# Performance work log

Hardware: AMD Instinct MI355X
Metric: run time of the kernel (lower is better)

The kernel has to match this reference:

```python
import jax, jax.numpy as jnp
import numpy as np
import math

D_MODEL = 512
N_HEADS = 8
MAX_SEQ_LEN = 4096
DENSITY = 0.3


def _make_random_mask(key, seq_len, density=DENSITY):
    # rand < density, symmetrized via (m + m.T)/2, clamped to [0,1], diag = 1
    u = jax.random.uniform(key, (seq_len, seq_len), dtype=jnp.float32)
    m = (u < density).astype(jnp.float32)
    m = jnp.clip((m + m.T) * 0.5, 0.0, 1.0)
    return m.at[jnp.diag_indices(seq_len)].set(1.0)


def setup_inputs() -> dict:
    key = jax.random.key(0)
    ks = jax.random.split(key, 10)
    B, T, C = 2, 4096, D_MODEL
    scale = 1.0 / math.sqrt(C)
    x = jax.random.normal(ks[0], (B, T, C), dtype=jnp.float32)
    mask = _make_random_mask(ks[1], MAX_SEQ_LEN)[:T, :T]
    # Linear weights stored as (in, out): y = x @ W + b
    Wq = jax.random.normal(ks[2], (C, C), dtype=jnp.float32) * scale
    Wk = jax.random.normal(ks[3], (C, C), dtype=jnp.float32) * scale
    Wv = jax.random.normal(ks[4], (C, C), dtype=jnp.float32) * scale
    Wo = jax.random.normal(ks[5], (C, C), dtype=jnp.float32) * scale
    bq = jax.random.normal(ks[6], (C,), dtype=jnp.float32) * scale
    bk = jax.random.normal(ks[7], (C,), dtype=jnp.float32) * scale
    bv = jax.random.normal(ks[8], (C,), dtype=jnp.float32) * scale
    bo = jax.random.normal(ks[9], (C,), dtype=jnp.float32) * scale
    return {"x": x, "mask": mask, "Wq": Wq, "bq": bq, "Wk": Wk, "bk": bk,
            "Wv": Wv, "bv": bv, "Wo": Wo, "bo": bo}


def reference(x, mask, Wq, bq, Wk, bk, Wv, bv, Wo, bo):
    B, T, C = x.shape
    H = N_HEADS
    dk = C // H
    q = (x @ Wq + bq).reshape(B, T, H, dk)
    k = (x @ Wk + bk).reshape(B, T, H, dk)
    v = (x @ Wv + bv).reshape(B, T, H, dk)
    # scores: [B, H, T, T]
    attn = jnp.einsum('bthd,bshd->bhts', q, k) / math.sqrt(dk)
    attn = attn * mask[None, None, :, :]  # multiplicative mask PRE-softmax
    p = jax.nn.softmax(attn, axis=-1)
    out = jnp.einsum('bhts,bshd->bthd', p, v).reshape(B, T, C)
    return out @ Wo + bo
```

## Files before the change

kernel.cpp:

```cpp
#include <hip/hip_runtime.h>
#include <math.h>

#define D_MODEL 512
#define N_HEADS 8
#define DK 64

typedef __attribute__((ext_vector_type(8))) short short8;
typedef __attribute__((ext_vector_type(4))) float f32x4;

typedef __attribute__((address_space(1))) const unsigned as1_uint;
typedef __attribute__((address_space(3))) unsigned as3_uint;

__device__ __forceinline__ unsigned short f2bf(float f) {
    unsigned u = __builtin_bit_cast(unsigned, f);
    u = (u + 0x7fff + ((u >> 16) & 1)) >> 16;
    return (unsigned short)u;
}

__global__ __launch_bounds__(256) void cvt_x_kernel(const float* __restrict__ x,
                                                    unsigned short* __restrict__ xb, int n8)
{
    int i = blockIdx.x * 256 + threadIdx.x;
    if (i >= n8) return;
    float4 a = ((const float4*)x)[i * 2];
    float4 b = ((const float4*)x)[i * 2 + 1];
    short8 o;
    o[0] = f2bf(a.x); o[1] = f2bf(a.y); o[2] = f2bf(a.z); o[3] = f2bf(a.w);
    o[4] = f2bf(b.x); o[5] = f2bf(b.y); o[6] = f2bf(b.z); o[7] = f2bf(b.w);
    ((short8*)xb)[i] = o;
}

__global__ __launch_bounds__(256) void cvt_wt_kernel(const float* __restrict__ W,
                                                     unsigned short* __restrict__ Wt)
{
    __shared__ float tile[64][65];
    int t = threadIdx.x;
    int c0 = blockIdx.x * 64;
    int r0 = blockIdx.y * 64;
    #pragma unroll
    for (int i = 0; i < 16; i++) {
        int e = i * 256 + t, r = e >> 6, c = e & 63;
        tile[c][r] = W[(size_t)(r0 + r) * D_MODEL + c0 + c];
    }
    __syncthreads();
    #pragma unroll
    for (int i = 0; i < 16; i++) {
        int e = i * 256 + t, n = e >> 6, kk = e & 63;
        Wt[(size_t)(c0 + n) * D_MODEL + r0 + kk] = f2bf(tile[n][kk]);
    }
}

template<int MODE>
__global__ __launch_bounds__(512) void gemm_mfma_kernel(
    const unsigned short* __restrict__ A, const unsigned short* __restrict__ Bt,
    const float* __restrict__ bias, void* __restrict__ outp, int M, int T)
{
    constexpr int K = D_MODEL;
    __shared__ unsigned short As[2][128 * 32];
    __shared__ unsigned short Bs[2][128 * 32];
    int t = threadIdx.x;
    int lane = t & 63, w = t >> 6;
    int ql = lane & 15, kg = lane >> 4;
    int m0 = blockIdx.y * 128, n0 = blockIdx.x * 128;
    int wm = w >> 2, wn = w & 3;

    const unsigned short* srcA = A + (size_t)(m0 + (t >> 2)) * K + (t & 3) * 8;
    const unsigned short* srcB = Bt + (size_t)(n0 + (t >> 2)) * K + (t & 3) * 8;

    f32x4 acc[4][2];
    #pragma unroll
    for (int i = 0; i < 4; i++)
        #pragma unroll
        for (int j = 0; j < 2; j++) { f32x4 z = {0.f, 0.f, 0.f, 0.f}; acc[i][j] = z; }

    constexpr int NIT = K / 32;
    int cur = 0;
    __builtin_amdgcn_global_load_lds((as1_uint*)(srcA),
        (as3_uint*)((char*)&As[0][0] + w * 1024), 16, 0, 0);
    __builtin_amdgcn_global_load_lds((as1_uint*)(srcB),
        (as3_uint*)((char*)&Bs[0][0] + w * 1024), 16, 0, 0);
    __syncthreads();

    for (int it = 0; it < NIT; ++it) {
        if (it + 1 < NIT) {
            int k0 = (it + 1) * 32;
            __builtin_amdgcn_global_load_lds((as1_uint*)(srcA + k0),
                (as3_uint*)((char*)&As[cur ^ 1][0] + w * 1024), 16, 0, 0);
            __builtin_amdgcn_global_load_lds((as1_uint*)(srcB + k0),
                (as3_uint*)((char*)&Bs[cur ^ 1][0] + w * 1024), 16, 0, 0);
        }
        short8 af[4], bfr[2];
        #pragma unroll
        for (int fm = 0; fm < 4; fm++)
            af[fm] = *(const short8*)((const char*)&As[cur][0] + (wm * 64 + fm * 16 + ql) * 64 + kg * 16);
        #pragma unroll
        for (int fn = 0; fn < 2; fn++)
            bfr[fn] = *(const short8*)((const char*)&Bs[cur][0] + (wn * 32 + fn * 16 + ql) * 64 + kg * 16);
        #pragma unroll
        for (int fm = 0; fm < 4; fm++)
            #pragma unroll
            for (int fn = 0; fn < 2; fn++) {
                if (MODE == 3)
                    acc[fm][fn] = __builtin_amdgcn_mfma_f32_16x16x32_bf16(bfr[fn], af[fm], acc[fm][fn], 0, 0, 0);
                else
                    acc[fm][fn] = __builtin_amdgcn_mfma_f32_16x16x32_bf16(af[fm], bfr[fn], acc[fm][fn], 0, 0, 0);
            }
        __syncthreads();
        cur ^= 1;
    }

    #pragma unroll
    for (int fm = 0; fm < 4; fm++) {
        #pragma unroll
        for (int fn = 0; fn < 2; fn++) {
            if (MODE == 3) {
                int m = m0 + wm * 64 + fm * 16 + ql;
                int b = m / T, tt = m % T;
                #pragma unroll
                for (int r = 0; r < 4; r++) {
                    int n = n0 + wn * 32 + fn * 16 + kg * 4 + r;
                    float val = acc[fm][fn][r] + bias[n];
                    int h = n >> 6, d = n & 63;
                    ((unsigned short*)outp)[((size_t)(b * N_HEADS + h) * DK + d) * T + tt] = f2bf(val);
                }
            } else {
                int n = n0 + wn * 32 + fn * 16 + ql;
                float bn = bias[n];
                #pragma unroll
                for (int r = 0; r < 4; r++) {
                    int m = m0 + wm * 64 + fm * 16 + kg * 4 + r;
                    float val = acc[fm][fn][r] + bn;
                    if (MODE == 0) {
                        ((float*)outp)[(size_t)m * D_MODEL + n] = val;
                    } else {
                        if (MODE == 1) val *= 0.125f * 1.44269504089f;
                        int b = m / T, tt = m % T;
                        int h = n >> 6, d = n & 63;
                        ((unsigned short*)outp)[((size_t)(b * N_HEADS + h) * T + tt) * DK + d] = f2bf(val);
                    }
                }
            }
        }
    }
}

__global__ __launch_bounds__(256) void attn_mfma_kernel(
    const unsigned short* __restrict__ q, const unsigned short* __restrict__ k,
    const unsigned short* __restrict__ v, const float* __restrict__ mask,
    unsigned short* __restrict__ out, int B, int T)
{
    __shared__ unsigned short Ks[2][64 * 64];
    __shared__ unsigned short Vt[2][64 * 64];
    __shared__ unsigned short Ps[4][16 * 64];

    int t = threadIdx.x;
    int lane = t & 63, w = t >> 6;
    int ql = lane & 15, kg = lane >> 4;
    int bh = blockIdx.x;
    int qt = blockIdx.y;
    int h = bh & (N_HEADS - 1), b = bh >> 3;
    int qr0 = qt * 64;

    const char* kbase = (const char*)(k + (size_t)bh * T * DK);
    const char* vbase = (const char*)(v + (size_t)bh * DK * T);
    const float* mrow = mask + (size_t)(qr0 + w * 16 + ql) * T + kg * 4;

    short8 qf[2];
    {
        const unsigned short* qrow = q + ((size_t)bh * T + qr0 + w * 16 + ql) * DK + kg * 8;
        qf[0] = *(const short8*)(qrow);
        qf[1] = *(const short8*)(qrow + 32);
    }

    f32x4 oacc[4];
    #pragma unroll
    for (int c = 0; c < 4; c++) { f32x4 z = {0.f, 0.f, 0.f, 0.f}; oacc[c] = z; }
    float lacc = 0.f;

    #pragma unroll
    for (int i = 0; i < 2; i++) {
        int off = (i * 256 + t) * 16;
        int row = off >> 7;
        short8 kv = *(const short8*)(kbase + off);
        short8 vv = *(const short8*)(vbase + (size_t)row * (T * 2) + (off & 127));
        *(short8*)((char*)&Ks[0][0] + (off ^ ((row & 7) << 4))) = kv;
        *(short8*)((char*)&Vt[0][0] + (off ^ ((row & 7) << 4))) = vv;
    }

    int ntiles = T / 64;
    for (int kt = 0; kt < ntiles; kt++) {
        __syncthreads();
        int cur = kt & 1;
        bool havenext = (kt + 1) < ntiles;

        float4 mv[4];
        const float* mp = mrow + (size_t)kt * 64;
        #pragma unroll
        for (int c = 0; c < 4; c++) mv[c] = *(const float4*)(mp + c * 16);

        short8 kreg[2], vreg[2];
        if (havenext) {
            #pragma unroll
            for (int i = 0; i < 2; i++) {
                int off = (i * 256 + t) * 16;
                int row = off >> 7;
                kreg[i] = *(const short8*)(kbase + (size_t)(kt + 1) * 8192 + off);
                vreg[i] = *(const short8*)(vbase + (size_t)row * (T * 2) + (size_t)(kt + 1) * 128 + (off & 127));
            }
        }

        f32x4 sacc[4];
        #pragma unroll
        for (int c = 0; c < 4; c++) { f32x4 z = {0.f, 0.f, 0.f, 0.f}; sacc[c] = z; }
        __builtin_amdgcn_s_setprio(1);
        #pragma unroll
        for (int ks = 0; ks < 2; ks++) {
            #pragma unroll
            for (int c = 0; c < 4; c++) {
                int row = c * 16 + ql;
                short8 kf = *(const short8*)((const char*)&Ks[cur][0] +
                            ((row * 128 + ks * 64 + kg * 16) ^ ((row & 7) << 4)));
                sacc[c] = __builtin_amdgcn_mfma_f32_16x16x32_bf16(kf, qf[ks], sacc[c], 0, 0, 0);
            }
        }
        __builtin_amdgcn_s_setprio(0);

        #pragma unroll
        for (int c = 0; c < 4; c++) {
            float p0 = __builtin_amdgcn_exp2f(sacc[c][0] * mv[c].x);
            float p1 = __builtin_amdgcn_exp2f(sacc[c][1] * mv[c].y);
            float p2 = __builtin_amdgcn_exp2f(sacc[c][2] * mv[c].z);
            float p3 = __builtin_amdgcn_exp2f(sacc[c][3] * mv[c].w);
            lacc += (p0 + p1) + (p2 + p3);
            unsigned lo, hi;
            asm("v_cvt_pk_bf16_f32 %0, %1, %2" : "=v"(lo) : "v"(p0), "v"(p1));
            asm("v_cvt_pk_bf16_f32 %0, %1, %2" : "=v"(hi) : "v"(p2), "v"(p3));
            int byteoff = (ql * 128 + (c * 16 + kg * 4) * 2) ^ ((ql & 7) << 4);
            uint2 pr = { lo, hi };
            *(uint2*)((char*)&Ps[w][0] + byteoff) = pr;
        }

        __builtin_amdgcn_s_setprio(1);
        #pragma unroll
        for (int ks = 0; ks < 2; ks++) {
            short8 pa = *(const short8*)((const char*)&Ps[w][0] +
                        ((ql * 128 + ks * 64 + kg * 16) ^ ((ql & 7) << 4)));
            #pragma unroll
            for (int c2 = 0; c2 < 4; c2++) {
                int rowd = c2 * 16 + ql;
                short8 vb = *(const short8*)((const char*)&Vt[cur][0] +
                            ((rowd * 128 + ks * 64 + kg * 16) ^ ((rowd & 7) << 4)));
                oacc[c2] = __builtin_amdgcn_mfma_f32_16x16x32_bf16(pa, vb, oacc[c2], 0, 0, 0);
            }
        }
        __builtin_amdgcn_s_setprio(0);

        if (havenext) {
            #pragma unroll
            for (int i = 0; i < 2; i++) {
                int off = (i * 256 + t) * 16;
                int row = off >> 7;
                *(short8*)((char*)&Ks[cur ^ 1][0] + (off ^ ((row & 7) << 4))) = kreg[i];
                *(short8*)((char*)&Vt[cur ^ 1][0] + (off ^ ((row & 7) << 4))) = vreg[i];
            }
        }
    }

    lacc += __shfl_xor(lacc, 16, 64);
    lacc += __shfl_xor(lacc, 32, 64);
    float linv[4];
    #pragma unroll
    for (int r = 0; r < 4; r++) linv[r] = 1.0f / __shfl(lacc, kg * 4 + r, 64);
    #pragma unroll
    for (int r = 0; r < 4; r++) {
        size_t rowo = ((size_t)b * T + qr0 + w * 16 + kg * 4 + r) * D_MODEL + h * DK;
        #pragma unroll
        for (int c2 = 0; c2 < 4; c2++)
            out[rowo + c2 * 16 + ql] = f2bf(oacc[c2][r] * linv[r]);
    }
}

extern "C" void kernel_launch(void* const* d_in, const int* in_sizes, int n_in,
                              void* d_out, int out_size, void* d_ws, size_t ws_size,
                              hipStream_t stream) {
    const float* x    = (const float*)d_in[0];
    const float* mask = (const float*)d_in[1];
    const float* Wq   = (const float*)d_in[2];
    const float* bq   = (const float*)d_in[3];
    const float* Wk   = (const float*)d_in[4];
    const float* bk   = (const float*)d_in[5];
    const float* Wv   = (const float*)d_in[6];
    const float* bv   = (const float*)d_in[7];
    const float* Wo   = (const float*)d_in[8];
    const float* bo   = (const float*)d_in[9];

    int T = (int)(sqrt((double)in_sizes[1]) + 0.5);
    int C = D_MODEL;
    int B = in_sizes[0] / (T * C);
    int M = B * T;

    size_t MK = (size_t)M * C;
    unsigned short* xb  = (unsigned short*)d_ws;
    unsigned short* Wtq = xb + MK;
    unsigned short* Wtk = Wtq + (size_t)C * C;
    unsigned short* Wtv = Wtk + (size_t)C * C;
    unsigned short* Wto = Wtv + (size_t)C * C;
    unsigned short* qb  = Wto + (size_t)C * C;
    unsigned short* kb  = qb + MK;
    unsigned short* vb  = kb + MK;
    unsigned short* attb = vb + MK;

    int n8 = (int)(MK / 8);
    cvt_x_kernel<<<(n8 + 255) / 256, 256, 0, stream>>>(x, xb, n8);
    dim3 wtg(C / 64, C / 64, 1);
    cvt_wt_kernel<<<wtg, 256, 0, stream>>>(Wq, Wtq);
    cvt_wt_kernel<<<wtg, 256, 0, stream>>>(Wk, Wtk);
    cvt_wt_kernel<<<wtg, 256, 0, stream>>>(Wv, Wtv);
    cvt_wt_kernel<<<wtg, 256, 0, stream>>>(Wo, Wto);

    dim3 gg(C / 128, M / 128, 1);
    gemm_mfma_kernel<1><<<gg, 512, 0, stream>>>(xb, Wtq, bq, qb, M, T);
    gemm_mfma_kernel<2><<<gg, 512, 0, stream>>>(xb, Wtk, bk, kb, M, T);
    gemm_mfma_kernel<3><<<gg, 512, 0, stream>>>(xb, Wtv, bv, vb, M, T);

    dim3 ga(B * N_HEADS, T / 64, 1);
    attn_mfma_kernel<<<ga, 256, 0, stream>>>(qb, kb, vb, mask, attb, B, T);

    gemm_mfma_kernel<0><<<gg, 512, 0, stream>>>(attb, Wto, bo, d_out, M, T);
}
```

Before: 241.7 us.

## Double query rows per attention block and stream K/V tiles directly into LDS

Each wave now handles 32 query rows instead of 16, so every K/V tile loaded into shared memory feeds twice as many MFMAs and global K/V traffic per output row is halved. The grid along the query dimension shrinks by two. K/V prefetch now uses global_load_lds direct-to-LDS loads with pre-swizzled source addresses instead of register staging and LDS stores. The trade-off is fewer blocks (occupancy and load balance across CUs), more registers for the doubled accumulators, and twice the mask loads per wave. Correctness of the async LDS loads depends on the existing __syncthreads ordering.

```diff
diff --git a/kernel.cpp b/kernel.cpp
--- a/kernel.cpp
+++ b/kernel.cpp
@@ -151,7 +151,7 @@
 {
     __shared__ unsigned short Ks[2][64 * 64];
     __shared__ unsigned short Vt[2][64 * 64];
-    __shared__ unsigned short Ps[4][16 * 64];
+    __shared__ unsigned short Ps[4][32 * 64];
 
     int t = threadIdx.x;
     int lane = t & 63, w = t >> 6;
@@ -159,59 +159,77 @@
     int bh = blockIdx.x;
     int qt = blockIdx.y;
     int h = bh & (N_HEADS - 1), b = bh >> 3;
-    int qr0 = qt * 64;
+    int qr0 = qt * 128;
 
     const char* kbase = (const char*)(k + (size_t)bh * T * DK);
     const char* vbase = (const char*)(v + (size_t)bh * DK * T);
-    const float* mrow = mask + (size_t)(qr0 + w * 16 + ql) * T + kg * 4;
-
-    short8 qf[2];
-    {
-        const unsigned short* qrow = q + ((size_t)bh * T + qr0 + w * 16 + ql) * DK + kg * 8;
-        qf[0] = *(const short8*)(qrow);
-        qf[1] = *(const short8*)(qrow + 32);
-    }
-
-    f32x4 oacc[4];
-    #pragma unroll
-    for (int c = 0; c < 4; c++) { f32x4 z = {0.f, 0.f, 0.f, 0.f}; oacc[c] = z; }
-    float lacc = 0.f;
-
-    #pragma unroll
-    for (int i = 0; i < 2; i++) {
-        int off = (i * 256 + t) * 16;
-        int row = off >> 7;
-        short8 kv = *(const short8*)(kbase + off);
-        short8 vv = *(const short8*)(vbase + (size_t)row * (T * 2) + (off & 127));
-        *(short8*)((char*)&Ks[0][0] + (off ^ ((row & 7) << 4))) = kv;
-        *(short8*)((char*)&Vt[0][0] + (off ^ ((row & 7) << 4))) = vv;
-    }
+
+    int lin0 = w * 1024 + lane * 16;
+    int lin1 = 4096 + lin0;
+    int row0 = lin0 >> 7, row1 = lin1 >> 7;
+    int sw0 = (row0 & 7) << 4, sw1 = (row1 & 7) << 4;
+    const char* gK0 = kbase + (lin0 ^ sw0);
+    const char* gK1 = kbase + (lin1 ^ sw1);
+    const char* gV0 = vbase + (size_t)row0 * (2 * T) + ((lin0 & 127) ^ sw0);
+    const char* gV1 = vbase + (size_t)row1 * (2 * T) + ((lin1 & 127) ^ sw1);
+
+    short8 qfr[2][2];
+    #pragma unroll
+    for (int qf = 0; qf < 2; qf++) {
+        const unsigned short* qrow = q + ((size_t)bh * T + qr0 + w * 32 + qf * 16 + ql) * DK + kg * 8;
+        qfr[qf][0] = *(const short8*)(qrow);
+        qfr[qf][1] = *(const short8*)(qrow + 32);
+    }
+
+    const float* mrow0 = mask + (size_t)(qr0 + w * 32 + ql) * T + kg * 4;
+    const float* mrow1 = mrow0 + (size_t)16 * T;
+
+    f32x4 oacc[2][4];
+    #pragma unroll
+    for (int qf = 0; qf < 2; qf++)
+        #pragma unroll
+        for (int c = 0; c < 4; c++) { f32x4 z = {0.f, 0.f, 0.f, 0.f}; oacc[qf][c] = z; }
+    float lacc0 = 0.f, lacc1 = 0.f;
+
+    __builtin_amdgcn_global_load_lds((as1_uint*)gK0, (as3_uint*)((char*)&Ks[0][0] + w * 1024), 16, 0, 0);
+    __builtin_amdgcn_global_load_lds((as1_uint*)gK1, (as3_uint*)((char*)&Ks[0][0] + 4096 + w * 1024), 16, 0, 0);
+    __builtin_amdgcn_global_load_lds((as1_uint*)gV0, (as3_uint*)((char*)&Vt[0][0] + w * 1024), 16, 0, 0);
+    __builtin_amdgcn_global_load_lds((as1_uint*)gV1, (as3_uint*)((char*)&Vt[0][0] + 4096 + w * 1024), 16, 0, 0);
 
     int ntiles = T / 64;
     for (int kt = 0; kt < ntiles; kt++) {
         __syncthreads();
         int cur = kt & 1;
-        bool havenext = (kt + 1) < ntiles;
-
-        float4 mv[4];
-        const float* mp = mrow + (size_t)kt * 64;
-        #pragma unroll
-        for (int c = 0; c < 4; c++) mv[c] = *(const float4*)(mp + c * 16);
-
-        short8 kreg[2], vreg[2];
-        if (havenext) {
-            #pragma unroll
-            for (int i = 0; i < 2; i++) {
-                int off = (i * 256 + t) * 16;
-                int row = off >> 7;
-                kreg[i] = *(const short8*)(kbase + (size_t)(kt + 1) * 8192 + off);
-                vreg[i] = *(const short8*)(vbase + (size_t)row * (T * 2) + (size_t)(kt + 1) * 128 + (off & 127));
-            }
-        }
-
-        f32x4 sacc[4];
-        #pragma unroll
-        for (int c = 0; c < 4; c++) { f32x4 z = {0.f, 0.f, 0.f, 0.f}; sacc[c] = z; }
+
+        float4 mv0[4], mv1[4];
+        {
+            const float* mp0 = mrow0 + (size_t)kt * 64;
+            const float* mp1 = mrow1 + (size_t)kt * 64;
+            #pragma unroll
+            for (int c = 0; c < 4; c++) {
+                mv0[c] = *(const float4*)(mp0 + c * 16);
+                mv1[c] = *(const float4*)(mp1 + c * 16);
+            }
+        }
+
+        if (kt + 1 < ntiles) {
+            size_t ko = (size_t)(kt + 1) * 8192;
+            size_t vo = (size_t)(kt + 1) * 128;
+            __builtin_amdgcn_global_load_lds((as1_uint*)(gK0 + ko),
+                (as3_uint*)((char*)&Ks[cur ^ 1][0] + w * 1024), 16, 0, 0);
+            __builtin_amdgcn_global_load_lds((as1_uint*)(gK1 + ko),
+                (as3_uint*)((char*)&Ks[cur ^ 1][0] + 4096 + w * 1024), 16, 0, 0);
+            __builtin_amdgcn_global_load_lds((as1_uint*)(gV0 + vo),
+                (as3_uint*)((char*)&Vt[cur ^ 1][0] + w * 1024), 16, 0, 0);
+            __builtin_amdgcn_global_load_lds((as1_uint*)(gV1 + vo),
+                (as3_uint*)((char*)&Vt[cur ^ 1][0] + 4096 + w * 1024), 16, 0, 0);
+        }
+
+        f32x4 sacc[2][4];
+        #pragma unroll
+        for (int qf = 0; qf < 2; qf++)
+            #pragma unroll
+            for (int c = 0; c < 4; c++) { f32x4 z = {0.f, 0.f, 0.f, 0.f}; sacc[qf][c] = z; }
         __builtin_amdgcn_s_setprio(1);
         #pragma unroll
         for (int ks = 0; ks < 2; ks++) {
@@ -220,63 +238,71 @@
                 int row = c * 16 + ql;
                 short8 kf = *(const short8*)((const char*)&Ks[cur][0] +
                             ((row * 128 + ks * 64 + kg * 16) ^ ((row & 7) << 4)));
-                sacc[c] = __builtin_amdgcn_mfma_f32_16x16x32_bf16(kf, qf[ks], sacc[c], 0, 0, 0);
+                sacc[0][c] = __builtin_amdgcn_mfma_f32_16x16x32_bf16(kf, qfr[0][ks], sacc[0][c], 0, 0, 0);
+                sacc[1][c] = __builtin_amdgcn_mfma_f32_16x16x32_bf16(kf, qfr[1][ks], sacc[1][c], 0, 0, 0);
             }
         }
         __builtin_amdgcn_s_setprio(0);
 
         #pragma unroll
         for (int c = 0; c < 4; c++) {
-            float p0 = __builtin_amdgcn_exp2f(sacc[c][0] * mv[c].x);
-            float p1 = __builtin_amdgcn_exp2f(sacc[c][1] * mv[c].y);
-            float p2 = __builtin_amdgcn_exp2f(sacc[c][2] * mv[c].z);
-            float p3 = __builtin_amdgcn_exp2f(sacc[c][3] * mv[c].w);
-            lacc += (p0 + p1) + (p2 + p3);
+            float p0 = __builtin_amdgcn_exp2f(sacc[0][c][0] * mv0[c].x);
+            float p1 = __builtin_amdgcn_exp2f(sacc[0][c][1] * mv0[c].y);
+            float p2 = __builtin_amdgcn_exp2f(sacc[0][c][2] * mv0[c].z);
+            float p3 = __builtin_amdgcn_exp2f(sacc[0][c][3] * mv0[c].w);
+            lacc0 += (p0 + p1) + (p2 + p3);
             unsigned lo, hi;
             asm("v_cvt_pk_bf16_f32 %0, %1, %2" : "=v"(lo) : "v"(p0), "v"(p1));
             asm("v_cvt_pk_bf16_f32 %0, %1, %2" : "=v"(hi) : "v"(p2), "v"(p3));
             int byteoff = (ql * 128 + (c * 16 + kg * 4) * 2) ^ ((ql & 7) << 4);
             uint2 pr = { lo, hi };
             *(uint2*)((char*)&Ps[w][0] + byteoff) = pr;
+
+            float q0 = __builtin_amdgcn_exp2f(sacc[1][c][0] * mv1[c].x);
+            float q1 = __builtin_amdgcn_exp2f(sacc[1][c][1] * mv1[c].y);
+            float q2 = __builtin_amdgcn_exp2f(sacc[1][c][2] * mv1[c].z);
+            float q3 = __builtin_amdgcn_exp2f(sacc[1][c][3] * mv1[c].w);
+            lacc1 += (q0 + q1) + (q2 + q3);
+            unsigned lo1, hi1;
+            asm("v_cvt_pk_bf16_f32 %0, %1, %2" : "=v"(lo1) : "v"(q0), "v"(q1));
+            asm("v_cvt_pk_bf16_f32 %0, %1, %2" : "=v"(hi1) : "v"(q2), "v"(q3));
+            uint2 pr1 = { lo1, hi1 };
+            *(uint2*)((char*)&Ps[w][0] + 2048 + byteoff) = pr1;
         }
 
         __builtin_amdgcn_s_setprio(1);
         #pragma unroll
         for (int ks = 0; ks < 2; ks++) {
-            short8 pa = *(const short8*)((const char*)&Ps[w][0] +
-                        ((ql * 128 + ks * 64 + kg * 16) ^ ((ql & 7) << 4)));
+            int pboff = (ql * 128 + ks * 64 + kg * 16) ^ ((ql & 7) << 4);
+            short8 pa0 = *(const short8*)((const char*)&Ps[w][0] + pboff);
+            short8 pa1 = *(const short8*)((const char*)&Ps[w][0] + 2048 + pboff);
             #pragma unroll
             for (int c2 = 0; c2 < 4; c2++) {
                 int rowd = c2 * 16 + ql;
                 short8 vb = *(const short8*)((const char*)&Vt[cur][0] +
                             ((rowd * 128 + ks * 64 + kg * 16) ^ ((rowd & 7) << 4)));
-                oacc[c2] = __builtin_amdgcn_mfma_f32_16x16x32_bf16(pa, vb, oacc[c2], 0, 0, 0);
+                oacc[0][c2] = __builtin_amdgcn_mfma_f32_16x16x32_bf16(pa0, vb, oacc[0][c2], 0, 0, 0);
+                oacc[1][c2] = __builtin_amdgcn_mfma_f32_16x16x32_bf16(pa1, vb, oacc[1][c2], 0, 0, 0);
             }
         }
         __builtin_amdgcn_s_setprio(0);
-
-        if (havenext) {
-            #pragma unroll
-            for (int i = 0; i < 2; i++) {
-                int off = (i * 256 + t) * 16;
-                int row = off >> 7;
-                *(short8*)((char*)&Ks[cur ^ 1][0] + (off ^ ((row & 7) << 4))) = kreg[i];
-                *(short8*)((char*)&Vt[cur ^ 1][0] + (off ^ ((row & 7) << 4))) = vreg[i];
-            }
-        }
-    }
-
-    lacc += __shfl_xor(lacc, 16, 64);
-    lacc += __shfl_xor(lacc, 32, 64);
-    float linv[4];
-    #pragma unroll
-    for (int r = 0; r < 4; r++) linv[r] = 1.0f / __shfl(lacc, kg * 4 + r, 64);
-    #pragma unroll
-    for (int r = 0; r < 4; r++) {
-        size_t rowo = ((size_t)b * T + qr0 + w * 16 + kg * 4 + r) * D_MODEL + h * DK;
-        #pragma unroll
-        for (int c2 = 0; c2 < 4; c2++)
-            out[rowo + c2 * 16 + ql] = f2bf(oacc[c2][r] * linv[r]);
+    }
+
+    lacc0 += __shfl_xor(lacc0, 16, 64);
+    lacc0 += __shfl_xor(lacc0, 32, 64);
+    lacc1 += __shfl_xor(lacc1, 16, 64);
+    lacc1 += __shfl_xor(lacc1, 32, 64);
+    #pragma unroll
+    for (int qf = 0; qf < 2; qf++) {
+        float la = qf ? lacc1 : lacc0;
+        #pragma unroll
+        for (int r = 0; r < 4; r++) {
+            float linv = 1.0f / __shfl(la, kg * 4 + r, 64);
+            size_t rowo = ((size_t)b * T + qr0 + w * 32 + qf * 16 + kg * 4 + r) * D_MODEL + h * DK;
+            #pragma unroll
+            for (int c2 = 0; c2 < 4; c2++)
+                out[rowo + c2 * 16 + ql] = f2bf(oacc[qf][c2][r] * linv);
+        }
     }
 }
 
@@ -323,7 +349,7 @@
     gemm_mfma_kernel<2><<<gg, 512, 0, stream>>>(xb, Wtk, bk, kb, M, T);
     gemm_mfma_kernel<3><<<gg, 512, 0, stream>>>(xb, Wtv, bv, vb, M, T);
 
-    dim3 ga(B * N_HEADS, T / 64, 1);
+    dim3 ga(B * N_HEADS, T / 128, 1);
     attn_mfma_kernel<<<ga, 256, 0, stream>>>(qb, kb, vb, mask, attb, B, T);
 
     gemm_mfma_kernel<0><<<gg, 512, 0, stream>>>(attb, Wto, bo, d_out, M, T);
```

Measured after the change: 230.7 us. 4.6% less time.
